# Performance work log

Hardware: AMD Instinct MI355X
Metric: run time of the kernel (lower is better)

The kernel has to match this reference:

```python
import jax, jax.numpy as jnp
import numpy as np
from jax import lax

V, D, H, C = 32000, 300, 300, 3
B, T = 128, 512


def setup_inputs() -> dict:
    key = jax.random.key(0)
    ks = jax.random.split(key, 8)
    sentence_ids = jax.random.randint(ks[0], (B, T), 0, V, dtype=jnp.int32)
    lengths = jnp.maximum(jax.random.randint(ks[1], (B,), 0, T, dtype=jnp.int32), 1)
    labels = jax.random.randint(ks[2], (B,), 0, C, dtype=jnp.int32)
    embedding = jax.random.normal(ks[3], (V, D), jnp.float32) * 0.1
    W_lstm = jax.random.normal(ks[4], (D + H, 4 * H), jnp.float32) * 0.05
    b_lstm = jnp.zeros((4 * H,), jnp.float32)
    W_dense = jax.random.normal(ks[5], (H, C), jnp.float32) * 0.05
    b_dense = jnp.zeros((C,), jnp.float32)
    return {"sentence_ids": sentence_ids, "lengths": lengths, "labels": labels,
            "embedding": embedding, "W_lstm": W_lstm, "b_lstm": b_lstm,
            "W_dense": W_dense, "b_dense": b_dense}


def reference(sentence_ids, lengths, labels, embedding, W_lstm, b_lstm, W_dense, b_dense):
    # Embedding lookup: [B, T, D]
    x = embedding[sentence_ids]
    b, t, d = x.shape
    h_units = W_dense.shape[0]
    FORGET_BIAS = 1.0  # TF BasicLSTMCell default

    xs = jnp.swapaxes(x, 0, 1)                                   # [T, B, D]
    step_mask = (jnp.arange(t)[:, None] < lengths[None, :])      # [T, B]

    def step(carry, inp):
        h, c = carry
        xt, m = inp                                              # [B,D], [B]
        z = jnp.concatenate([xt, h], axis=-1) @ W_lstm + b_lstm  # [B, 4H]
        i, j, f, o = jnp.split(z, 4, axis=-1)
        new_c = c * jax.nn.sigmoid(f + FORGET_BIAS) + jax.nn.sigmoid(i) * jnp.tanh(j)
        new_h = jnp.tanh(new_c) * jax.nn.sigmoid(o)
        mm = m[:, None]
        # dynamic_rnn: freeze state past each sequence's length
        h = jnp.where(mm, new_h, h)
        c = jnp.where(mm, new_c, c)
        return (h, c), None

    h0 = jnp.zeros((b, h_units), x.dtype)
    c0 = jnp.zeros((b, h_units), x.dtype)
    (h_final, _), _ = lax.scan(step, (h0, c0), (xs, step_mask))

    logits = h_final @ W_dense + b_dense                          # [B, C]
    logp = jax.nn.log_softmax(logits, axis=-1)
    nll = -jnp.take_along_axis(logp, labels[:, None].astype(jnp.int32), axis=1)[:, 0]
    loss = jnp.mean(nll)
    return loss, logits
```

## Files before the change

kernel.cpp:

```cpp
#include <hip/hip_runtime.h>
#include <hip/hip_bf16.h>
#include <math.h>

#define VV   32000
#define DD   300
#define HU   300
#define NC   3
#define BB   128
#define TT   512
#define N4H  1200
#define CHUNK 64
#define NCHUNK (TT / CHUNK)

#define GC   15
#define GR   16
#define RPW  8
#define UPW  20
#define KSW  96
#define HLB_STRIDE 312
#define HLB_SIZE   (16 * HLB_STRIDE + 32)

static constexpr size_t ZX_F   = (size_t)BB * CHUNK * N4H;
static constexpr size_t EX_W   = (size_t)2 * GR * RPW * HU;
static constexpr size_t CST_F  = (size_t)BB * HU;
static constexpr size_t HFIN_F = (size_t)BB * HU;

typedef __attribute__((ext_vector_type(8))) short bf16x8;
typedef __attribute__((ext_vector_type(8))) _Float16 f16x8;
typedef __attribute__((ext_vector_type(4))) float f32x4;
typedef unsigned long long ull;

__device__ __forceinline__ short f2bf(float f) {
    unsigned u = __float_as_uint(f);
    u += 0x7fff + ((u >> 16) & 1);
    return (short)(u >> 16);
}
__device__ __forceinline__ short f2h(float f) {
    _Float16 h = (_Float16)f;
    return *(short*)&h;
}
__device__ __forceinline__ float h2f(short s) {
    _Float16 h = *(_Float16*)&s;
    return (float)h;
}
__device__ __forceinline__ float sigm(float x) { return 1.f / (1.f + __expf(-x)); }
__device__ __forceinline__ float tanh_(float x) { return 1.f - 2.f / (__expf(2.f * x) + 1.f); }

__global__ void init_kernel(ull* __restrict__ ex, float* __restrict__ cst,
                            float* __restrict__ out) {
    size_t i = (size_t)blockIdx.x * 256 + threadIdx.x;
    if (i < EX_W) ex[i] = 0ull;
    if (i < CST_F) cst[i] = 0.f;
    if (i == 0) out[0] = 0.f;
}

__global__ __launch_bounds__(256) void zx_gemm(
    const float* __restrict__ emb, const int* __restrict__ ids,
    const float* __restrict__ Wl, const float* __restrict__ bl,
    float* __restrict__ zx, int t0)
{
    __shared__ short A_l[256 * 40];
    __shared__ short B_l[80 * 40];
    __shared__ int   ids_l[256];

    const int tid = threadIdx.x;
    const int m0  = blockIdx.x * 256;
    const int n0  = blockIdx.y * 80;
    const int wv  = tid >> 6, ln = tid & 63;

    {
        int m = m0 + tid;
        int b = m >> 6, tc = m & (CHUNK - 1);
        ids_l[tid] = ids[b * TT + t0 + tc];
    }

    f32x4 acc[4][5];
    for (int i = 0; i < 4; ++i)
        for (int j = 0; j < 5; ++j)
            acc[i][j] = (f32x4){0.f, 0.f, 0.f, 0.f};

    for (int k0 = 0; k0 < 320; k0 += 32) {
        __syncthreads();
        {
            const float* src = emb + (size_t)ids_l[tid] * DD;
            #pragma unroll
            for (int q = 0; q < 8; ++q) {
                int kg = k0 + q * 4;
                float4 v;
                if (kg < DD) v = *(const float4*)(src + kg);
                else         v = make_float4(0.f, 0.f, 0.f, 0.f);
                short4 s; s.x = f2bf(v.x); s.y = f2bf(v.y); s.z = f2bf(v.z); s.w = f2bf(v.w);
                *(short4*)&A_l[tid * 40 + q * 4] = s;
            }
        }
        {
            int kk = tid >> 3;
            int c0 = (tid & 7) * 10;
            int kg = k0 + kk;
            #pragma unroll
            for (int c = 0; c < 10; ++c) {
                float v = (kg < DD) ? Wl[(size_t)kg * N4H + n0 + c0 + c] : 0.f;
                B_l[(c0 + c) * 40 + kk] = f2bf(v);
            }
        }
        __syncthreads();
        const int koff = (ln >> 4) * 8;
        bf16x8 afr[4], bfr[5];
        #pragma unroll
        for (int mt = 0; mt < 4; ++mt) {
            int row = wv * 64 + mt * 16 + (ln & 15);
            afr[mt] = *(const bf16x8*)&A_l[row * 40 + koff];
        }
        #pragma unroll
        for (int nt = 0; nt < 5; ++nt) {
            int col = nt * 16 + (ln & 15);
            bfr[nt] = *(const bf16x8*)&B_l[col * 40 + koff];
        }
        #pragma unroll
        for (int mt = 0; mt < 4; ++mt)
            #pragma unroll
            for (int nt = 0; nt < 5; ++nt)
                acc[mt][nt] = __builtin_amdgcn_mfma_f32_16x16x32_bf16(
                    afr[mt], bfr[nt], acc[mt][nt], 0, 0, 0);
    }
    #pragma unroll
    for (int mt = 0; mt < 4; ++mt) {
        #pragma unroll
        for (int nt = 0; nt < 5; ++nt) {
            #pragma unroll
            for (int rg = 0; rg < 4; ++rg) {
                int row = m0 + wv * 64 + mt * 16 + (ln >> 4) * 4 + rg;
                int col = n0 + nt * 16 + (ln & 15);
                zx[(size_t)row * N4H + col] = acc[mt][nt][rg] + bl[col];
            }
        }
    }
}

__global__ __launch_bounds__(256, 1) void lstm_rec(
    const float* __restrict__ zx, const float* __restrict__ Wl,
    const int* __restrict__ lens, ull* __restrict__ ex,
    float* __restrict__ cst, float* __restrict__ hfin, int t0)
{
    const int tid = threadIdx.x;
    const int wv  = tid >> 6, ln = tid & 63;
    const int rg  = blockIdx.x % GR;
    const int cgi = blockIdx.x / GR;
    const int r0  = rg * RPW;
    const int u0  = cgi * UPW;
    const int m   = ln & 15;
    const int quad = ln >> 4;

    const int pstart_tbl[4] = {0, 4, 9, 14};
    const int np_tbl[4]     = {5, 6, 6, 1};
    const int pstart = pstart_tbl[wv];
    const int np     = np_tbl[wv];

    __shared__ short h_hi[HLB_SIZE];
    __shared__ short h_lo[HLB_SIZE];
    __shared__ float zp[2][4][RPW][84];
    __shared__ short w_l[4 * 15 * 64 * 8];

    #pragma unroll
    for (int s = 0; s < 3; ++s) {
        #pragma unroll
        for (int nt = 0; nt < 5; ++nt) {
            int c    = nt * 16 + m;
            int gate = c / 20;
            int wcol = 300 * gate + u0 + (c % 20);
            f16x8 b;
            #pragma unroll
            for (int j = 0; j < 8; ++j) {
                int k = KSW * wv + 32 * s + quad * 8 + j;
                float v = (k < HU) ? Wl[(size_t)(DD + k) * N4H + wcol] : 0.f;
                b[j] = (_Float16)v;
            }
            *(f16x8*)&w_l[(((wv * 15) + (s * 5 + nt)) * 64 + ln) * 8] = b;
        }
    }
    const int nks = (wv == 3) ? 1 : 3;

    for (int i = tid; i < HLB_SIZE; i += 256) { h_hi[i] = 0; h_lo[i] = 0; }

    const int g_u = tid % UPW, g_r = tid / UPW;
    const bool gl = (tid < RPW * UPW);
    float c_reg = 0.f, ho_reg = 0.f;
    int mylen = 0;
    if (gl) {
        c_reg = cst[(size_t)(r0 + g_r) * HU + u0 + g_u];
        mylen = lens[r0 + g_r];
        if (t0 > 0) {
            ull v = __hip_atomic_load(
                ex + (((size_t)(t0 & 1) * GR + rg) * RPW + g_r) * HU + u0 + g_u,
                __ATOMIC_RELAXED, __HIP_MEMORY_SCOPE_AGENT);
            ho_reg = __uint_as_float((unsigned)v);
        }
    }
    __syncthreads();

    for (int tc = 0; tc < CHUNK; ++tc) {
        const int t = t0 + tc;
        const int par = t & 1;

        float z_pre[4];
        if (gl) {
            const float* zrow = zx + ((size_t)(r0 + g_r) * CHUNK + tc) * N4H;
            #pragma unroll
            for (int gg = 0; gg < 4; ++gg)
                z_pre[gg] = zrow[300 * gg + u0 + g_u];
        }

        if (t > 0) {
            const ull* exb = ex + ((size_t)par * GR + rg) * (RPW * HU);

            if (ln < np) {
                const ull* sp = exb + (pstart + ln) * UPW;
                while ((int)(__hip_atomic_load(sp, __ATOMIC_RELAXED,
                             __HIP_MEMORY_SCOPE_AGENT) >> 32) < t)
                    __builtin_amdgcn_s_sleep(1);
            }

            if (wv < 3) {
                unsigned pend = 0xFFFu;
                do {
                    ull v[12];
                    #pragma unroll
                    for (int k = 0; k < 12; ++k)
                        if ((pend >> k) & 1) {
                            int i = ln + (k << 6);
                            int r = i / 96, u = KSW * wv + (i % 96);
                            v[k] = __hip_atomic_load(exb + r * HU + u,
                                                     __ATOMIC_RELAXED,
                                                     __HIP_MEMORY_SCOPE_AGENT);
                        }
                    unsigned got = 0;
                    #pragma unroll
                    for (int k = 0; k < 12; ++k) {
                        if (((pend >> k) & 1) && (int)(v[k] >> 32) >= t) {
                            int i = ln + (k << 6);
                            int r = i / 96, u = KSW * wv + (i % 96);
                            int idx = r * HLB_STRIDE + u;
                            float f = __uint_as_float((unsigned)v[k]);
                            short hi = f2h(f);
                            h_hi[idx] = hi;
                            h_lo[idx] = f2h(f - h2f(hi));
                            got |= 1u << k;
                        }
                    }
                    pend &= ~got;
                    if (pend) __builtin_amdgcn_s_sleep(1);
                } while (pend);
            } else {
                unsigned pend = (ln < 32) ? 0x3u : 0x1u;
                do {
                    ull v[2];
                    #pragma unroll
                    for (int k = 0; k < 2; ++k)
                        if ((pend >> k) & 1) {
                            int i = ln + (k << 6);
                            int r = i / 12, u = 288 + (i % 12);
                            v[k] = __hip_atomic_load(exb + r * HU + u,
                                                     __ATOMIC_RELAXED,
                                                     __HIP_MEMORY_SCOPE_AGENT);
                        }
                    unsigned got = 0;
                    #pragma unroll
                    for (int k = 0; k < 2; ++k) {
                        if (((pend >> k) & 1) && (int)(v[k] >> 32) >= t) {
                            int i = ln + (k << 6);
                            int r = i / 12, u = 288 + (i % 12);
                            int idx = r * HLB_STRIDE + u;
                            float f = __uint_as_float((unsigned)v[k]);
                            short hi = f2h(f);
                            h_hi[idx] = hi;
                            h_lo[idx] = f2h(f - h2f(hi));
                            got |= 1u << k;
                        }
                    }
                    pend &= ~got;
                    if (pend) __builtin_amdgcn_s_sleep(1);
                } while (pend);
            }
        }

        f32x4 acc[5];
        #pragma unroll
        for (int nt = 0; nt < 5; ++nt) acc[nt] = (f32x4){0.f, 0.f, 0.f, 0.f};
        for (int s = 0; s < nks; ++s) {
            const int aoff = m * HLB_STRIDE + KSW * wv + 32 * s + quad * 8;
            f16x8 ah = *(const f16x8*)&h_hi[aoff];
            f16x8 al = *(const f16x8*)&h_lo[aoff];
            f16x8 bfr[5];
            #pragma unroll
            for (int nt = 0; nt < 5; ++nt)
                bfr[nt] = *(const f16x8*)&w_l[(((wv * 15) + (s * 5 + nt)) * 64 + ln) * 8];
            #pragma unroll
            for (int nt = 0; nt < 5; ++nt)
                acc[nt] = __builtin_amdgcn_mfma_f32_16x16x32_f16(
                    ah, bfr[nt], acc[nt], 0, 0, 0);
            #pragma unroll
            for (int nt = 0; nt < 5; ++nt)
                acc[nt] = __builtin_amdgcn_mfma_f32_16x16x32_f16(
                    al, bfr[nt], acc[nt], 0, 0, 0);
        }
        if (ln < 32) {
            #pragma unroll
            for (int nt = 0; nt < 5; ++nt)
                #pragma unroll
                for (int r4 = 0; r4 < 4; ++r4)
                    zp[par][wv][quad * 4 + r4][nt * 16 + m] = acc[nt][r4];
        }
        __syncthreads();

        if (gl) {
            const int b = r0 + g_r;
            float z4[4];
            #pragma unroll
            for (int gg = 0; gg < 4; ++gg) {
                int cidx = gg * UPW + g_u;
                z4[gg] = z_pre[gg] + zp[par][0][g_r][cidx] + zp[par][1][g_r][cidx]
                                   + zp[par][2][g_r][cidx] + zp[par][3][g_r][cidx];
            }
            float ig = sigm(z4[0]);
            float jg = tanh_(z4[1]);
            float fg = sigm(z4[2] + 1.0f);
            float og = sigm(z4[3]);
            float c_new = c_reg * fg + ig * jg;
            float h_new = tanh_(c_new) * og;
            bool upd = (t < mylen);
            ho_reg = upd ? h_new : ho_reg;
            c_reg  = upd ? c_new : c_reg;
            ull pk = ((ull)(unsigned)(t + 1) << 32) | (ull)__float_as_uint(ho_reg);
            __hip_atomic_store(
                ex + (((size_t)((t + 1) & 1) * GR + rg) * RPW + g_r) * HU + u0 + g_u,
                pk, __ATOMIC_RELAXED, __HIP_MEMORY_SCOPE_AGENT);
            if (tc == CHUNK - 1) hfin[(size_t)b * HU + u0 + g_u] = ho_reg;
        }
    }
    if (gl) cst[(size_t)(r0 + g_r) * HU + u0 + g_u] = c_reg;
}

__global__ __launch_bounds__(64) void cls_kernel(
    const float* __restrict__ hfin, const float* __restrict__ Wd,
    const float* __restrict__ bd, const int* __restrict__ labels,
    float* __restrict__ out)
{
    const int b = blockIdx.x;
    const int ln = threadIdx.x;
    const float* h = hfin + (size_t)b * HU;
    float p0 = 0.f, p1 = 0.f, p2 = 0.f;
    for (int k = ln; k < HU; k += 64) {
        float hv = h[k];
        p0 += hv * Wd[k * 3 + 0];
        p1 += hv * Wd[k * 3 + 1];
        p2 += hv * Wd[k * 3 + 2];
    }
    #pragma unroll
    for (int off = 32; off > 0; off >>= 1) {
        p0 += __shfl_down(p0, off);
        p1 += __shfl_down(p1, off);
        p2 += __shfl_down(p2, off);
    }
    if (ln == 0) {
        float l0 = p0 + bd[0], l1 = p1 + bd[1], l2 = p2 + bd[2];
        float m = fmaxf(l0, fmaxf(l1, l2));
        float lse = m + logf(__expf(l0 - m) + __expf(l1 - m) + __expf(l2 - m));
        int lab = labels[b];
        float sel = (lab == 0) ? l0 : ((lab == 1) ? l1 : l2);
        float nll = lse - sel;
        out[1 + b * 3 + 0] = l0;
        out[1 + b * 3 + 1] = l1;
        out[1 + b * 3 + 2] = l2;
        atomicAdd(out, nll * (1.0f / BB));
    }
}

extern "C" void kernel_launch(void* const* d_in, const int* in_sizes, int n_in,
                              void* d_out, int out_size, void* d_ws, size_t ws_size,
                              hipStream_t stream) {
    const int*   ids  = (const int*)d_in[0];
    const int*   lens = (const int*)d_in[1];
    const int*   labs = (const int*)d_in[2];
    const float* emb  = (const float*)d_in[3];
    const float* Wl   = (const float*)d_in[4];
    const float* bl   = (const float*)d_in[5];
    const float* Wd   = (const float*)d_in[6];
    const float* bd   = (const float*)d_in[7];
    float* out = (float*)d_out;

    float* zx   = (float*)d_ws;
    ull*   ex   = (ull*)(zx + ZX_F);
    float* cst  = (float*)(ex + EX_W);
    float* hfin = cst + CST_F;

    {
        int n = (int)((EX_W + 255) / 256);
        init_kernel<<<n, 256, 0, stream>>>(ex, cst, out);
    }
    for (int c = 0; c < NCHUNK; ++c) {
        int t0 = c * CHUNK;
        zx_gemm<<<dim3(32, 15), 256, 0, stream>>>(emb, ids, Wl, bl, zx, t0);
        lstm_rec<<<GR * GC, 256, 0, stream>>>(zx, Wl, lens, ex, cst, hfin, t0);
    }
    cls_kernel<<<BB, 64, 0, stream>>>(hfin, Wd, bd, labs, out);
}
```

Baseline: 2.309 ms.

## Replace tagged 64-bit hidden-state exchange with packed fp16 pairs and per-wave flags

```diff
diff --git a/kernel.cpp b/kernel.cpp
--- a/kernel.cpp
+++ b/kernel.cpp
@@ -21,7 +21,8 @@
 #define HLB_SIZE   (16 * HLB_STRIDE + 32)
 
 static constexpr size_t ZX_F   = (size_t)BB * CHUNK * N4H;
-static constexpr size_t EX_W   = (size_t)2 * GR * RPW * HU;
+static constexpr size_t EXV_W  = (size_t)2 * GR * RPW * HU;
+static constexpr size_t EXT_W  = (size_t)2 * GR * GC * 4;
 static constexpr size_t CST_F  = (size_t)BB * HU;
 static constexpr size_t HFIN_F = (size_t)BB * HU;
 
@@ -46,10 +47,10 @@
 __device__ __forceinline__ float sigm(float x) { return 1.f / (1.f + __expf(-x)); }
 __device__ __forceinline__ float tanh_(float x) { return 1.f - 2.f / (__expf(2.f * x) + 1.f); }
 
-__global__ void init_kernel(ull* __restrict__ ex, float* __restrict__ cst,
+__global__ void init_kernel(unsigned* __restrict__ ext, float* __restrict__ cst,
                             float* __restrict__ out) {
     size_t i = (size_t)blockIdx.x * 256 + threadIdx.x;
-    if (i < EX_W) ex[i] = 0ull;
+    if (i < EXT_W) ext[i] = 0u;
     if (i < CST_F) cst[i] = 0.f;
     if (i == 0) out[0] = 0.f;
 }
@@ -139,8 +140,9 @@
 
 __global__ __launch_bounds__(256, 1) void lstm_rec(
     const float* __restrict__ zx, const float* __restrict__ Wl,
-    const int* __restrict__ lens, ull* __restrict__ ex,
-    float* __restrict__ cst, float* __restrict__ hfin, int t0)
+    const int* __restrict__ lens, unsigned* __restrict__ exv,
+    unsigned* __restrict__ ext, float* __restrict__ cst,
+    float* __restrict__ hfin, int t0)
 {
     const int tid = threadIdx.x;
     const int wv  = tid >> 6, ln = tid & 63;
@@ -156,8 +158,8 @@
     const int pstart = pstart_tbl[wv];
     const int np     = np_tbl[wv];
 
-    __shared__ short h_hi[HLB_SIZE];
-    __shared__ short h_lo[HLB_SIZE];
+    __shared__ __align__(16) short h_hi[HLB_SIZE];
+    __shared__ __align__(16) short h_lo[HLB_SIZE];
     __shared__ float zp[2][4][RPW][84];
     __shared__ short w_l[4 * 15 * 64 * 8];
 
@@ -190,10 +192,10 @@
         c_reg = cst[(size_t)(r0 + g_r) * HU + u0 + g_u];
         mylen = lens[r0 + g_r];
         if (t0 > 0) {
-            ull v = __hip_atomic_load(
-                ex + (((size_t)(t0 & 1) * GR + rg) * RPW + g_r) * HU + u0 + g_u,
+            unsigned v = __hip_atomic_load(
+                exv + (((size_t)(t0 & 1) * GR + rg) * RPW + g_r) * HU + u0 + g_u,
                 __ATOMIC_RELAXED, __HIP_MEMORY_SCOPE_AGENT);
-            ho_reg = __uint_as_float((unsigned)v);
+            ho_reg = h2f((short)(v & 0xFFFFu)) + h2f((short)(v >> 16));
         }
     }
     __syncthreads();
@@ -211,75 +213,47 @@
         }
 
         if (t > 0) {
-            const ull* exb = ex + ((size_t)par * GR + rg) * (RPW * HU);
-
-            if (ln < np) {
-                const ull* sp = exb + (pstart + ln) * UPW;
-                while ((int)(__hip_atomic_load(sp, __ATOMIC_RELAXED,
-                             __HIP_MEMORY_SCOPE_AGENT) >> 32) < t)
+            const unsigned* evb = exv + ((size_t)par * GR + rg) * (RPW * HU);
+            const unsigned* etb = ext + ((size_t)par * GR + rg) * (GC * 4);
+
+            if (ln < np * 3) {
+                int p = pstart + ln / 3;
+                int w = ln - 3 * (ln / 3);
+                const unsigned* tp = etb + p * 4 + w;
+                while (__hip_atomic_load(tp, __ATOMIC_RELAXED,
+                                         __HIP_MEMORY_SCOPE_AGENT) < (unsigned)t)
                     __builtin_amdgcn_s_sleep(1);
             }
 
             if (wv < 3) {
-                unsigned pend = 0xFFFu;
-                do {
-                    ull v[12];
-                    #pragma unroll
-                    for (int k = 0; k < 12; ++k)
-                        if ((pend >> k) & 1) {
-                            int i = ln + (k << 6);
-                            int r = i / 96, u = KSW * wv + (i % 96);
-                            v[k] = __hip_atomic_load(exb + r * HU + u,
-                                                     __ATOMIC_RELAXED,
-                                                     __HIP_MEMORY_SCOPE_AGENT);
-                        }
-                    unsigned got = 0;
-                    #pragma unroll
-                    for (int k = 0; k < 12; ++k) {
-                        if (((pend >> k) & 1) && (int)(v[k] >> 32) >= t) {
-                            int i = ln + (k << 6);
-                            int r = i / 96, u = KSW * wv + (i % 96);
-                            int idx = r * HLB_STRIDE + u;
-                            float f = __uint_as_float((unsigned)v[k]);
-                            short hi = f2h(f);
-                            h_hi[idx] = hi;
-                            h_lo[idx] = f2h(f - h2f(hi));
-                            got |= 1u << k;
-                        }
-                    }
-                    pend &= ~got;
-                    if (pend) __builtin_amdgcn_s_sleep(1);
-                } while (pend);
-            } else {
-                unsigned pend = (ln < 32) ? 0x3u : 0x1u;
-                do {
-                    ull v[2];
-                    #pragma unroll
-                    for (int k = 0; k < 2; ++k)
-                        if ((pend >> k) & 1) {
-                            int i = ln + (k << 6);
-                            int r = i / 12, u = 288 + (i % 12);
-                            v[k] = __hip_atomic_load(exb + r * HU + u,
-                                                     __ATOMIC_RELAXED,
-                                                     __HIP_MEMORY_SCOPE_AGENT);
-                        }
-                    unsigned got = 0;
-                    #pragma unroll
-                    for (int k = 0; k < 2; ++k) {
-                        if (((pend >> k) & 1) && (int)(v[k] >> 32) >= t) {
-                            int i = ln + (k << 6);
-                            int r = i / 12, u = 288 + (i % 12);
-                            int idx = r * HLB_STRIDE + u;
-                            float f = __uint_as_float((unsigned)v[k]);
-                            short hi = f2h(f);
-                            h_hi[idx] = hi;
-                            h_lo[idx] = f2h(f - h2f(hi));
-                            got |= 1u << k;
-                        }
-                    }
-                    pend &= ~got;
-                    if (pend) __builtin_amdgcn_s_sleep(1);
-                } while (pend);
+                ull v[6];
+                #pragma unroll
+                for (int k = 0; k < 6; ++k) {
+                    int i = 2 * ln + (k << 7);
+                    int r = i / 96, u = KSW * wv + (i % 96);
+                    v[k] = __hip_atomic_load((const ull*)(evb + r * HU + u),
+                                             __ATOMIC_RELAXED,
+                                             __HIP_MEMORY_SCOPE_AGENT);
+                }
+                #pragma unroll
+                for (int k = 0; k < 6; ++k) {
+                    int i = 2 * ln + (k << 7);
+                    int r = i / 96, u = KSW * wv + (i % 96);
+                    int idx = r * HLB_STRIDE + u;
+                    unsigned v0 = (unsigned)v[k], v1 = (unsigned)(v[k] >> 32);
+                    *(unsigned*)&h_hi[idx] = (v0 & 0xFFFFu) | (v1 << 16);
+                    *(unsigned*)&h_lo[idx] = (v0 >> 16) | (v1 & 0xFFFF0000u);
+                }
+            } else if (ln < 48) {
+                int i = 2 * ln;
+                int r = i / 12, u = 288 + (i % 12);
+                ull v = __hip_atomic_load((const ull*)(evb + r * HU + u),
+                                          __ATOMIC_RELAXED,
+                                          __HIP_MEMORY_SCOPE_AGENT);
+                int idx = r * HLB_STRIDE + u;
+                unsigned v0 = (unsigned)v, v1 = (unsigned)(v >> 32);
+                *(unsigned*)&h_hi[idx] = (v0 & 0xFFFFu) | (v1 << 16);
+                *(unsigned*)&h_lo[idx] = (v0 >> 16) | (v1 & 0xFFFF0000u);
             }
         }
 
@@ -330,11 +304,19 @@
             bool upd = (t < mylen);
             ho_reg = upd ? h_new : ho_reg;
             c_reg  = upd ? c_new : c_reg;
-            ull pk = ((ull)(unsigned)(t + 1) << 32) | (ull)__float_as_uint(ho_reg);
+            short hhi = f2h(ho_reg);
+            short hlo = f2h(ho_reg - h2f(hhi));
+            unsigned val = ((unsigned)(unsigned short)hlo << 16)
+                         | (unsigned)(unsigned short)hhi;
             __hip_atomic_store(
-                ex + (((size_t)((t + 1) & 1) * GR + rg) * RPW + g_r) * HU + u0 + g_u,
-                pk, __ATOMIC_RELAXED, __HIP_MEMORY_SCOPE_AGENT);
+                exv + (((size_t)((t + 1) & 1) * GR + rg) * RPW + g_r) * HU + u0 + g_u,
+                val, __ATOMIC_RELAXED, __HIP_MEMORY_SCOPE_AGENT);
             if (tc == CHUNK - 1) hfin[(size_t)b * HU + u0 + g_u] = ho_reg;
+            asm volatile("s_waitcnt vmcnt(0)" ::: "memory");
+            if (ln == 0)
+                __hip_atomic_store(
+                    ext + (((size_t)((t + 1) & 1) * GR + rg) * GC + cgi) * 4 + wv,
+                    (unsigned)(t + 1), __ATOMIC_RELAXED, __HIP_MEMORY_SCOPE_AGENT);
         }
     }
     if (gl) cst[(size_t)(r0 + g_r) * HU + u0 + g_u] = c_reg;
@@ -388,19 +370,20 @@
     const float* bd   = (const float*)d_in[7];
     float* out = (float*)d_out;
 
-    float* zx   = (float*)d_ws;
-    ull*   ex   = (ull*)(zx + ZX_F);
-    float* cst  = (float*)(ex + EX_W);
-    float* hfin = cst + CST_F;
+    float*    zx   = (float*)d_ws;
+    unsigned* exv  = (unsigned*)(zx + ZX_F);
+    unsigned* ext  = exv + EXV_W;
+    float*    cst  = (float*)(ext + EXT_W);
+    float*    hfin = cst + CST_F;
 
     {
-        int n = (int)((EX_W + 255) / 256);
-        init_kernel<<<n, 256, 0, stream>>>(ex, cst, out);
+        int n = (int)((CST_F + 255) / 256);
+        init_kernel<<<n, 256, 0, stream>>>(ext, cst, out);
     }
     for (int c = 0; c < NCHUNK; ++c) {
         int t0 = c * CHUNK;
         zx_gemm<<<dim3(32, 15), 256, 0, stream>>>(emb, ids, Wl, bl, zx, t0);
-        lstm_rec<<<GR * GC, 256, 0, stream>>>(zx, Wl, lens, ex, cst, hfin, t0);
+        lstm_rec<<<GR * GC, 256, 0, stream>>>(zx, Wl, lens, exv, ext, cst, hfin, t0);
     }
     cls_kernel<<<BB, 64, 0, stream>>>(hfin, Wd, bd, labs, out);
 }
```

Result: slower. 3.302 ms (+43.0%).
